# Performance work log

Measured on AMD Instinct MI355X. Metric: run time of the kernel, lower is better.

## Reference

```python
import jax, jax.numpy as jnp
import numpy as np

# Module hyperparameters (from init_kwargs)
KH = KW = 3
STRIDE = 2
PAD = 1
OUT_PAD = 1
DIL = 1
IN_LEN = 8   # length of each input capsule
OUT_LEN = 8  # length of each output capsule
N_IN_CAPS = 64 // IN_LEN    # 8
N_OUT_CAPS = 64 // OUT_LEN  # 8
NUM_ITERATIONS = 3


def _squash(x):
    # v * |v|^2 / ((1 + |v|^2) * |v|), along last (capsule-length) dim
    sn = jnp.sum(x * x, axis=-1, keepdims=True)
    return x * (sn / ((1.0 + sn) * jnp.sqrt(sn + 1e-12)))


def _k_means_routing(priors, num_iterations):
    # priors: [..., K, M] ; soft k-means routing with 'dot' similarity,
    # softmax over the votes dim K (softmax_dim=-2), squash at the end.
    out = jnp.mean(priors, axis=-2, keepdims=True)          # [..., 1, M]
    for _ in range(num_iterations):
        nrm = jnp.linalg.norm(out, axis=-1, keepdims=True)
        out_n = out / jnp.maximum(nrm, 1e-12)               # F.normalize(p=2)
        logits = jnp.sum(priors * out_n, axis=-1, keepdims=True)  # [..., K, 1]
        probs = jax.nn.softmax(logits, axis=-2)
        out = jnp.sum(probs * priors, axis=-2, keepdims=True)
    return _squash(out)[..., 0, :]                          # [..., M]


def setup_inputs() -> dict:
    key = jax.random.key(0)
    k1, k2, k3 = jax.random.split(key, 3)
    input = jax.random.normal(k1, (2, 64, 32, 32), dtype=jnp.float32)
    # weight: (in_length, out_channels//out_length, out_length, kh, kw)
    weight = jax.random.normal(k2, (IN_LEN, N_OUT_CAPS, OUT_LEN, KH, KW), dtype=jnp.float32) * 0.1
    # bias: (out_channels//out_length, out_length)
    bias = jax.random.normal(k3, (N_OUT_CAPS, OUT_LEN), dtype=jnp.float32) * 0.1
    return {"input": input, "weight": weight, "bias": bias}


def reference(input, weight, bias):
    n, c_in, h_in, w_in = input.shape
    fi = c_in // IN_LEN
    fo = weight.shape[1]
    # conv_transpose == conv(lhs-dilated input, spatially flipped kernel)
    pad_lo = DIL * (KH - 1) - PAD
    patches = jax.lax.conv_general_dilated_patches(
        input, (KH, KW), (1, 1),
        padding=((pad_lo, pad_lo + OUT_PAD), (pad_lo, pad_lo + OUT_PAD)),
        lhs_dilation=(STRIDE, STRIDE), rhs_dilation=(DIL, DIL))
    ho, wo = patches.shape[-2], patches.shape[-1]
    # feature dim of patches is ordered (c, kh, kw), channel-major
    patches = patches.reshape(n, fi, IN_LEN, KH, KW, ho, wo)
    w_flip = weight[..., ::-1, ::-1]  # [IN_LEN, fo, OUT_LEN, KH, KW]
    # votes: each (input capsule, kernel tap) casts a vote per output capsule
    priors = jnp.einsum('nflhwpq,lgmhw->npqgfhwm', patches, w_flip)
    priors = priors.reshape(n, ho, wo, fo, fi * KH * KW, OUT_LEN)
    out = _k_means_routing(priors, NUM_ITERATIONS)  # [n, ho, wo, fo, OUT_LEN]
    out = out + bias                                # bias: [fo, OUT_LEN]
    out = out.reshape(n, ho, wo, fo * OUT_LEN).transpose(0, 3, 1, 2)
    return out  # [n, out_channels, ho, wo] = [2, 64, 64, 64]
```

## Files before the change

### kernel.cpp

```cpp
#include <hip/hip_runtime.h>
#include <math.h>

#define HIN 32
#define WIN 32
#define NITER 3

typedef float f2 __attribute__((ext_vector_type(2)));
static __device__ __forceinline__ f2 mk2(float a, float b) { f2 r; r.x = a; r.y = b; return r; }
static __device__ __forceinline__ f2 fma2(f2 a, f2 b, f2 c) { return __builtin_elementwise_fma(a, b, c); }

template <int CTRL>
__device__ __forceinline__ float dpp_add(float v) {
    int p = __builtin_amdgcn_update_dpp(0, __float_as_int(v), CTRL, 0xF, 0xF, true);
    return v + __int_as_float(p);
}
__device__ __forceinline__ float sum8(float v) {
    v = dpp_add<0xB1>(v);
    v = dpp_add<0x4E>(v);
    v = dpp_add<0x141>(v);
    return v;
}

template <int TH, int TW>
__device__ __forceinline__ void stage_weights(const float* __restrict__ weight,
                                              float* __restrict__ wlds, int t) {
    constexpr int T = TH * TW;
    const int sg = (t >> 3) & 7;
    const int sm = t & 7;
    const int l0 = t >> 6;
    const int dbase = sg * 80 + (((sm >> 1) + sg) & 3) * 20 + (sm & 1);
#pragma unroll
    for (int k = 0; k < 2 * T; ++k) {
        const int vtap = k >> 1;
        const int chunk = k & 1;
        const int hh = (TH == 1) ? 1 : ((vtap / TW) * 2);
        const int ww = (TW == 1) ? 1 : ((vtap % TW) * 2);
        const int jflip = (2 - hh) * 3 + (2 - ww);
        const int l = chunk * 4 + l0;
        wlds[vtap * 640 + dbase + l * 2] = weight[(chunk * 256 + t) * 9 + jflip];
    }
}

template <int NROWS, int NCHUNK>
__device__ __forceinline__ void stage_input(const float* __restrict__ in,
                                            float* __restrict__ ilds,
                                            int t, int n, int y0, int x0) {
    const int c = t >> 2, r = t & 3;
#pragma unroll
    for (int pp = r; pp < NROWS * NCHUNK; pp += 4) {
        const int yi = pp / NCHUNK, ch = pp % NCHUNK;
        const int y = y0 + yi;
        const int xc = x0 + ch * 4;
        float4 vv = {0.f, 0.f, 0.f, 0.f};
        if (y < HIN && xc < WIN)
            vv = *(const float4*)(in + (((size_t)(n * 64 + c) * HIN + y) * WIN + xc));
        ilds[(yi * 12 + ch * 4 + 0) * 64 + c] = vv.x;
        ilds[(yi * 12 + ch * 4 + 1) * 64 + c] = vv.y;
        ilds[(yi * 12 + ch * 4 + 2) * 64 + c] = vv.z;
        ilds[(yi * 12 + ch * 4 + 3) * 64 + c] = vv.w;
    }
}

template <int TH, int TW>
__device__ __forceinline__ void compute_pri(const float* __restrict__ ilds,
                                            const float* __restrict__ wlds,
                                            int q, int x0, int pi, int g, int s,
                                            f2 (&pri2)[TH * TW][4]) {
#pragma unroll
    for (int i = 0; i < TH; ++i) {
        const int y = (TH == 1) ? pi : (pi + i);
        const bool vy = (y < HIN);
#pragma unroll
        for (int j = 0; j < TW; ++j) {
            const int v = i * TW + j;
            const int w = (TW == 1) ? 1 : j * 2;
            const int x = (q + w - 1) >> 1;
            if (vy && x < WIN) {
                const float4* xp =
                    (const float4*)(ilds + (i * 12 + (x - x0)) * 64 + s * 8);
                float4 x0v = xp[0], x1v = xp[1];
                float xv[8] = {x0v.x, x0v.y, x0v.z, x0v.w, x1v.x, x1v.y, x1v.z, x1v.w};
                const float* wb = wlds + v * 640 + g * 80;
#pragma unroll
                for (int m2 = 0; m2 < 4; ++m2) {
                    const float4* row = (const float4*)(wb + ((m2 + g) & 3) * 20);
                    f2 acc = mk2(0.f, 0.f);
#pragma unroll
                    for (int k = 0; k < 4; ++k) {
                        float4 w4 = row[k];
                        acc = fma2(mk2(xv[2 * k], xv[2 * k]), mk2(w4.x, w4.y), acc);
                        acc = fma2(mk2(xv[2 * k + 1], xv[2 * k + 1]), mk2(w4.z, w4.w), acc);
                    }
                    pri2[v][m2] = acc;
                }
            } else {
#pragma unroll
                for (int m2 = 0; m2 < 4; ++m2) pri2[v][m2] = mk2(0.f, 0.f);
            }
        }
    }
}

template <int T>
__device__ __forceinline__ float route_core(const f2 (&pri2)[T][4],
                                            const float* __restrict__ bias,
                                            int g, int s) {
    constexpr float Z = (float)(72 - 8 * T);
    f2 rr[4];
#pragma unroll
    for (int m2 = 0; m2 < 4; ++m2) {
        f2 a = mk2(0.f, 0.f);
#pragma unroll
        for (int v = 0; v < T; ++v) a += pri2[v][m2];
        rr[m2].x = sum8(a.x);
        rr[m2].y = sum8(a.y);
    }
    float r8v = 0.f;
#pragma unroll
    for (int it = 0; it < NITER; ++it) {
        f2 t2 = mk2(0.f, 0.f);
#pragma unroll
        for (int m2 = 0; m2 < 4; ++m2) t2 = fma2(rr[m2], rr[m2], t2);
        const float sn = t2.x + t2.y;
        const float inv = __builtin_amdgcn_rsqf(fmaxf(sn, 1e-24f));
        const f2 inv2 = mk2(inv, inv);
        f2 on2[4];
#pragma unroll
        for (int m2 = 0; m2 < 4; ++m2) on2[m2] = rr[m2] * inv2;

        float a8 = 0.f;
        f2 acc2[4];
#pragma unroll
        for (int m2 = 0; m2 < 4; ++m2) acc2[m2] = mk2(0.f, 0.f);
#pragma unroll
        for (int v = 0; v < T; ++v) {
            f2 d2 = mk2(0.f, 0.f);
#pragma unroll
            for (int m2 = 0; m2 < 4; ++m2) d2 = fma2(pri2[v][m2], on2[m2], d2);
            const float e = __expf(d2.x + d2.y);
            a8 += e;
            const f2 e2 = mk2(e, e);
#pragma unroll
            for (int m2 = 0; m2 < 4; ++m2) acc2[m2] = fma2(e2, pri2[v][m2], acc2[m2]);
        }
#pragma unroll
        for (int m2 = 0; m2 < 4; ++m2) {
            rr[m2].x = sum8(acc2[m2].x);
            rr[m2].y = sum8(acc2[m2].y);
        }
        if (it == NITER - 1) r8v = sum8(a8);
    }
    const float invs = __builtin_amdgcn_rcpf(r8v + Z);
    const f2 invs2 = mk2(invs, invs);
    f2 o2[4];
#pragma unroll
    for (int m2 = 0; m2 < 4; ++m2) o2[m2] = rr[m2] * invs2;
    f2 s2 = mk2(0.f, 0.f);
#pragma unroll
    for (int m2 = 0; m2 < 4; ++m2) s2 = fma2(o2[m2], o2[m2], s2);
    const float sn = s2.x + s2.y;
    const float factor =
        sn * __builtin_amdgcn_rcpf(1.f + sn) * __builtin_amdgcn_rsqf(sn + 1e-12f);
    f2 osel = o2[0];
#pragma unroll
    for (int m2 = 1; m2 < 4; ++m2)
        if ((s >> 1) == m2) osel = o2[m2];
    float val = (s & 1) ? osel.y : osel.x;
    return val * factor + bias[g * 8 + s];
}

template <int TH, int TW>
__device__ __forceinline__ void run_dual(
    const float* __restrict__ in, const float* __restrict__ weight,
    const float* __restrict__ bias, float* __restrict__ out,
    float* __restrict__ ilds, float* __restrict__ wlds, float* __restrict__ olds,
    int t, int n, int p, int pi, int qb, int x0) {
    constexpr int T = TH * TW;
    stage_input<TH, (TW == 2 ? 3 : 2)>(in, ilds, t, n, pi, x0);
    stage_weights<TH, TW>(weight, wlds, t);
    __syncthreads();

    const int wave = t >> 6;
    const int lane = t & 63;
    const int g = lane >> 3;
    const int s = lane & 7;
    const int qa = qb + 2 * wave;

    f2 pa[T][4], pb[T][4];
    compute_pri<TH, TW>(ilds, wlds, qa, x0, pi, g, s, pa);
    compute_pri<TH, TW>(ilds, wlds, qa + 8, x0, pi, g, s, pb);

    const float va = route_core<T>(pa, bias, g, s);
    const float vb = route_core<T>(pb, bias, g, s);

    olds[lane * 9 + wave] = va;
    olds[lane * 9 + wave + 4] = vb;
    __syncthreads();
    const int c2 = t >> 2, w = t & 3;
    float* ob = out + (((size_t)n * 64 + c2) * 64 + p) * 64 + qb;
    ob[2 * w] = olds[c2 * 9 + w];
    ob[2 * w + 8] = olds[c2 * 9 + w + 4];
}

__device__ __forceinline__ void run_t4(
    const float* __restrict__ in, const float* __restrict__ weight,
    const float* __restrict__ bias, float* __restrict__ out,
    float* __restrict__ ilds, float* __restrict__ wlds, float* __restrict__ olds,
    int t, int n, int p, int pi, int qb, int x0) {
    stage_input<2, 2>(in, ilds, t, n, pi, x0);
    stage_weights<2, 2>(weight, wlds, t);
    __syncthreads();

    const int wave = t >> 6;
    const int lane = t & 63;
    const int g = lane >> 3;
    const int s = lane & 7;

    f2 pa[4][4];
    compute_pri<2, 2>(ilds, wlds, qb + 2 * wave, x0, pi, g, s, pa);
    const float va = route_core<4>(pa, bias, g, s);

    olds[lane * 5 + wave] = va;
    __syncthreads();
    const int c2 = t >> 2, w = t & 3;
    out[(((size_t)n * 64 + c2) * 64 + p) * 64 + qb + 2 * w] = olds[c2 * 5 + w];
}

__global__ __launch_bounds__(256) void caps_routing(
    const float* __restrict__ in, const float* __restrict__ weight,
    const float* __restrict__ bias, float* __restrict__ out) {
    __shared__ float ilds[2 * 12 * 64];
    __shared__ float wlds[4 * 640];
    __shared__ float olds[576];
    const int t = threadIdx.x;

    const int b = blockIdx.x;
    const int grp = b / 5;
    const int sel = b - grp * 5;

    if (sel < 2) {
        const int idx = grp * 2 + sel;
        const int n = idx >> 8, r = idx & 255;
        const int pi = r >> 3, jq = r & 7;
        run_t4(in, weight, bias, out, ilds, wlds, olds,
               t, n, 2 * pi + 1, pi, 8 * jq + 1, 4 * jq);
    } else {
        const int n = grp >> 7, r = grp & 127;
        const int pi = r >> 2, jq = r & 3;
        if (sel == 2)
            run_dual<2, 1>(in, weight, bias, out, ilds, wlds, olds,
                           t, n, 2 * pi + 1, pi, 16 * jq, 8 * jq);
        else if (sel == 3)
            run_dual<1, 2>(in, weight, bias, out, ilds, wlds, olds,
                           t, n, 2 * pi, pi, 16 * jq + 1, 8 * jq);
        else
            run_dual<1, 1>(in, weight, bias, out, ilds, wlds, olds,
                           t, n, 2 * pi, pi, 16 * jq, 8 * jq);
    }
}

extern "C" void kernel_launch(void* const* d_in, const int* in_sizes, int n_in,
                              void* d_out, int out_size, void* d_ws, size_t ws_size,
                              hipStream_t stream) {
    const float* in = (const float*)d_in[0];
    const float* weight = (const float*)d_in[1];
    const float* bias = (const float*)d_in[2];
    float* out = (float*)d_out;
    (void)d_ws; (void)ws_size;

    caps_routing<<<1280, 256, 0, stream>>>(in, weight, bias, out);
}
```

Before: 66.76 us.

## Share weight loads across multiple pixels and rebalance block work mix

Compute priors for several output pixels per thread, loading each weight row once and reusing it across pixels. The single-tap class now handles four pixels per thread in new quad blocks, and the block schedule moves from 5 to 9 blocks per group for a grid of 1152. In-bounds checks in the prior computation are removed, which relies on zero-padded shared-memory staging and adds register pressure.

```diff
diff --git a/kernel.cpp b/kernel.cpp
--- a/kernel.cpp
+++ b/kernel.cpp
@@ -41,7 +41,7 @@
     }
 }
 
-template <int NROWS, int NCHUNK>
+template <int NROWS, int NCHUNK, int XW>
 __device__ __forceinline__ void stage_input(const float* __restrict__ in,
                                             float* __restrict__ ilds,
                                             int t, int n, int y0, int x0) {
@@ -54,48 +54,51 @@
         float4 vv = {0.f, 0.f, 0.f, 0.f};
         if (y < HIN && xc < WIN)
             vv = *(const float4*)(in + (((size_t)(n * 64 + c) * HIN + y) * WIN + xc));
-        ilds[(yi * 12 + ch * 4 + 0) * 64 + c] = vv.x;
-        ilds[(yi * 12 + ch * 4 + 1) * 64 + c] = vv.y;
-        ilds[(yi * 12 + ch * 4 + 2) * 64 + c] = vv.z;
-        ilds[(yi * 12 + ch * 4 + 3) * 64 + c] = vv.w;
-    }
-}
-
-template <int TH, int TW>
-__device__ __forceinline__ void compute_pri(const float* __restrict__ ilds,
-                                            const float* __restrict__ wlds,
-                                            int q, int x0, int pi, int g, int s,
-                                            f2 (&pri2)[TH * TW][4]) {
+        ilds[(yi * XW + ch * 4 + 0) * 64 + c] = vv.x;
+        ilds[(yi * XW + ch * 4 + 1) * 64 + c] = vv.y;
+        ilds[(yi * XW + ch * 4 + 2) * 64 + c] = vv.z;
+        ilds[(yi * XW + ch * 4 + 3) * 64 + c] = vv.w;
+    }
+}
+
+template <int TH, int TW, int NP, int XW>
+__device__ __forceinline__ void compute_pri_multi(const float* __restrict__ ilds,
+                                                  const float* __restrict__ wlds,
+                                                  int q0, int dq, int x0, int g, int s,
+                                                  f2 (&pri2)[NP][TH * TW][4]) {
 #pragma unroll
     for (int i = 0; i < TH; ++i) {
-        const int y = (TH == 1) ? pi : (pi + i);
-        const bool vy = (y < HIN);
 #pragma unroll
         for (int j = 0; j < TW; ++j) {
             const int v = i * TW + j;
-            const int w = (TW == 1) ? 1 : j * 2;
-            const int x = (q + w - 1) >> 1;
-            if (vy && x < WIN) {
-                const float4* xp =
-                    (const float4*)(ilds + (i * 12 + (x - x0)) * 64 + s * 8);
-                float4 x0v = xp[0], x1v = xp[1];
-                float xv[8] = {x0v.x, x0v.y, x0v.z, x0v.w, x1v.x, x1v.y, x1v.z, x1v.w};
-                const float* wb = wlds + v * 640 + g * 80;
-#pragma unroll
-                for (int m2 = 0; m2 < 4; ++m2) {
-                    const float4* row = (const float4*)(wb + ((m2 + g) & 3) * 20);
+            float xv[NP][8];
+#pragma unroll
+            for (int pp = 0; pp < NP; ++pp) {
+                const int w = (TW == 1) ? 1 : (j * 2);
+                const int xi = ((q0 + dq * pp + w - 1) >> 1) - x0;
+                const float4* xp = (const float4*)(ilds + (i * XW + xi) * 64 + s * 8);
+                float4 a = xp[0], b = xp[1];
+                xv[pp][0] = a.x; xv[pp][1] = a.y; xv[pp][2] = a.z; xv[pp][3] = a.w;
+                xv[pp][4] = b.x; xv[pp][5] = b.y; xv[pp][6] = b.z; xv[pp][7] = b.w;
+            }
+            const float* wb = wlds + v * 640 + g * 80;
+#pragma unroll
+            for (int m2 = 0; m2 < 4; ++m2) {
+                const float4* row = (const float4*)(wb + ((m2 + g) & 3) * 20);
+                float4 w0 = row[0], w1 = row[1], w2 = row[2], w3 = row[3];
+#pragma unroll
+                for (int pp = 0; pp < NP; ++pp) {
                     f2 acc = mk2(0.f, 0.f);
-#pragma unroll
-                    for (int k = 0; k < 4; ++k) {
-                        float4 w4 = row[k];
-                        acc = fma2(mk2(xv[2 * k], xv[2 * k]), mk2(w4.x, w4.y), acc);
-                        acc = fma2(mk2(xv[2 * k + 1], xv[2 * k + 1]), mk2(w4.z, w4.w), acc);
-                    }
-                    pri2[v][m2] = acc;
+                    acc = fma2(mk2(xv[pp][0], xv[pp][0]), mk2(w0.x, w0.y), acc);
+                    acc = fma2(mk2(xv[pp][1], xv[pp][1]), mk2(w0.z, w0.w), acc);
+                    acc = fma2(mk2(xv[pp][2], xv[pp][2]), mk2(w1.x, w1.y), acc);
+                    acc = fma2(mk2(xv[pp][3], xv[pp][3]), mk2(w1.z, w1.w), acc);
+                    acc = fma2(mk2(xv[pp][4], xv[pp][4]), mk2(w2.x, w2.y), acc);
+                    acc = fma2(mk2(xv[pp][5], xv[pp][5]), mk2(w2.z, w2.w), acc);
+                    acc = fma2(mk2(xv[pp][6], xv[pp][6]), mk2(w3.x, w3.y), acc);
+                    acc = fma2(mk2(xv[pp][7], xv[pp][7]), mk2(w3.z, w3.w), acc);
+                    pri2[pp][v][m2] = acc;
                 }
-            } else {
-#pragma unroll
-                for (int m2 = 0; m2 < 4; ++m2) pri2[v][m2] = mk2(0.f, 0.f);
             }
         }
     }
@@ -169,32 +172,38 @@
     return val * factor + bias[g * 8 + s];
 }
 
-template <int TH, int TW>
+__device__ __forceinline__ void run_t4(
+    const float* __restrict__ in, const float* __restrict__ weight,
+    const float* __restrict__ bias, float* __restrict__ out,
+    float* __restrict__ ilds, float* __restrict__ wlds, float* __restrict__ olds,
+    int t, int n, int p, int pi, int qb, int x0) {
+    stage_input<2, 2, 8>(in, ilds, t, n, pi, x0);
+    stage_weights<2, 2>(weight, wlds, t);
+    __syncthreads();
+    const int wave = t >> 6, lane = t & 63, g = lane >> 3, s = lane & 7;
+    f2 pa[1][4][4];
+    compute_pri_multi<2, 2, 1, 8>(ilds, wlds, qb + 2 * wave, 0, x0, g, s, pa);
+    olds[lane * 5 + wave] = route_core<4>(pa[0], bias, g, s);
+    __syncthreads();
+    const int c2 = t >> 2, w = t & 3;
+    out[(((size_t)n * 64 + c2) * 64 + p) * 64 + qb + 2 * w] = olds[c2 * 5 + w];
+}
+
+template <int TH, int TW, int XW>
 __device__ __forceinline__ void run_dual(
     const float* __restrict__ in, const float* __restrict__ weight,
     const float* __restrict__ bias, float* __restrict__ out,
     float* __restrict__ ilds, float* __restrict__ wlds, float* __restrict__ olds,
     int t, int n, int p, int pi, int qb, int x0) {
     constexpr int T = TH * TW;
-    stage_input<TH, (TW == 2 ? 3 : 2)>(in, ilds, t, n, pi, x0);
+    stage_input<TH, XW / 4, XW>(in, ilds, t, n, pi, x0);
     stage_weights<TH, TW>(weight, wlds, t);
     __syncthreads();
-
-    const int wave = t >> 6;
-    const int lane = t & 63;
-    const int g = lane >> 3;
-    const int s = lane & 7;
-    const int qa = qb + 2 * wave;
-
-    f2 pa[T][4], pb[T][4];
-    compute_pri<TH, TW>(ilds, wlds, qa, x0, pi, g, s, pa);
-    compute_pri<TH, TW>(ilds, wlds, qa + 8, x0, pi, g, s, pb);
-
-    const float va = route_core<T>(pa, bias, g, s);
-    const float vb = route_core<T>(pb, bias, g, s);
-
-    olds[lane * 9 + wave] = va;
-    olds[lane * 9 + wave + 4] = vb;
+    const int wave = t >> 6, lane = t & 63, g = lane >> 3, s = lane & 7;
+    f2 pp2[2][T][4];
+    compute_pri_multi<TH, TW, 2, XW>(ilds, wlds, qb + 2 * wave, 8, x0, g, s, pp2);
+    olds[lane * 9 + wave] = route_core<T>(pp2[0], bias, g, s);
+    olds[lane * 9 + wave + 4] = route_core<T>(pp2[1], bias, g, s);
     __syncthreads();
     const int c2 = t >> 2, w = t & 3;
     float* ob = out + (((size_t)n * 64 + c2) * 64 + p) * 64 + qb;
@@ -202,60 +211,60 @@
     ob[2 * w + 8] = olds[c2 * 9 + w + 4];
 }
 
-__device__ __forceinline__ void run_t4(
+__device__ __forceinline__ void run_quad1(
     const float* __restrict__ in, const float* __restrict__ weight,
     const float* __restrict__ bias, float* __restrict__ out,
     float* __restrict__ ilds, float* __restrict__ wlds, float* __restrict__ olds,
-    int t, int n, int p, int pi, int qb, int x0) {
-    stage_input<2, 2>(in, ilds, t, n, pi, x0);
-    stage_weights<2, 2>(weight, wlds, t);
-    __syncthreads();
-
-    const int wave = t >> 6;
-    const int lane = t & 63;
-    const int g = lane >> 3;
-    const int s = lane & 7;
-
-    f2 pa[4][4];
-    compute_pri<2, 2>(ilds, wlds, qb + 2 * wave, x0, pi, g, s, pa);
-    const float va = route_core<4>(pa, bias, g, s);
-
-    olds[lane * 5 + wave] = va;
+    int t, int n, int p, int pi, int q0, int x0) {
+    stage_input<1, 4, 16>(in, ilds, t, n, pi, x0);
+    stage_weights<1, 1>(weight, wlds, t);
+    __syncthreads();
+    const int wave = t >> 6, lane = t & 63, g = lane >> 3, s = lane & 7;
+    f2 pq[4][1][4];
+    compute_pri_multi<1, 1, 4, 16>(ilds, wlds, q0 + 8 * wave, 2, x0, g, s, pq);
+#pragma unroll
+    for (int k = 0; k < 4; ++k)
+        olds[lane * 17 + wave * 4 + k] = route_core<1>(pq[k], bias, g, s);
     __syncthreads();
     const int c2 = t >> 2, w = t & 3;
-    out[(((size_t)n * 64 + c2) * 64 + p) * 64 + qb + 2 * w] = olds[c2 * 5 + w];
+    float* ob = out + (((size_t)n * 64 + c2) * 64 + p) * 64 + q0 + 8 * w;
+#pragma unroll
+    for (int k = 0; k < 4; ++k) ob[2 * k] = olds[c2 * 17 + 4 * w + k];
 }
 
 __global__ __launch_bounds__(256) void caps_routing(
     const float* __restrict__ in, const float* __restrict__ weight,
     const float* __restrict__ bias, float* __restrict__ out) {
-    __shared__ float ilds[2 * 12 * 64];
+    __shared__ float ilds[16 * 64];
     __shared__ float wlds[4 * 640];
-    __shared__ float olds[576];
+    __shared__ float olds[64 * 17];
     const int t = threadIdx.x;
 
     const int b = blockIdx.x;
-    const int grp = b / 5;
-    const int sel = b - grp * 5;
-
-    if (sel < 2) {
-        const int idx = grp * 2 + sel;
+    const int grp = b / 9;
+    const int sel = b - grp * 9;
+
+    if (sel < 4) {
+        const int idx = grp * 4 + sel;
         const int n = idx >> 8, r = idx & 255;
         const int pi = r >> 3, jq = r & 7;
         run_t4(in, weight, bias, out, ilds, wlds, olds,
                t, n, 2 * pi + 1, pi, 8 * jq + 1, 4 * jq);
+    } else if (sel < 8) {
+        const int idx = grp * 2 + (sel & 1);
+        const int n = idx >> 7, r = idx & 127;
+        const int pi = r >> 2, jq = r & 3;
+        if (sel < 6)
+            run_dual<2, 1, 8>(in, weight, bias, out, ilds, wlds, olds,
+                              t, n, 2 * pi + 1, pi, 16 * jq, 8 * jq);
+        else
+            run_dual<1, 2, 12>(in, weight, bias, out, ilds, wlds, olds,
+                               t, n, 2 * pi, pi, 16 * jq + 1, 8 * jq);
     } else {
-        const int n = grp >> 7, r = grp & 127;
-        const int pi = r >> 2, jq = r & 3;
-        if (sel == 2)
-            run_dual<2, 1>(in, weight, bias, out, ilds, wlds, olds,
-                           t, n, 2 * pi + 1, pi, 16 * jq, 8 * jq);
-        else if (sel == 3)
-            run_dual<1, 2>(in, weight, bias, out, ilds, wlds, olds,
-                           t, n, 2 * pi, pi, 16 * jq + 1, 8 * jq);
-        else
-            run_dual<1, 1>(in, weight, bias, out, ilds, wlds, olds,
-                           t, n, 2 * pi, pi, 16 * jq, 8 * jq);
+        const int n = grp >> 6, r = grp & 63;
+        const int pi = r >> 1, jh = r & 1;
+        run_quad1(in, weight, bias, out, ilds, wlds, olds,
+                  t, n, 2 * pi, pi, 32 * jh, 16 * jh);
     }
 }
 
@@ -268,5 +277,5 @@
     float* out = (float*)d_out;
     (void)d_ws; (void)ws_size;
 
-    caps_routing<<<1280, 256, 0, stream>>>(in, weight, bias, out);
-}
+    caps_routing<<<1152, 256, 0, stream>>>(in, weight, bias, out);
+}
```

Result: no change. 67.05 us (+0.4%).
